# Optimization experiments

Hardware: AMD Instinct MI355X
Metric: run time of the kernel (lower is better)

The kernel has to match this reference:

```python
import jax, jax.numpy as jnp
import numpy as np

D_MODEL = 64
D_INNER = 128
D_STATE = 16
D_CONV = 4
DT_RANK = 4
P_PIX = 5
HH = 120
WW = 120


def _layernorm(x, g, b):
    m = x.mean(-1, keepdims=True)
    v = ((x - m) ** 2).mean(-1, keepdims=True)
    return (x - m) * jax.lax.rsqrt(v + 1e-5) * g + b


def _ssm_scan(delta, Bm, Cm, u, A):
    # delta,u: (b,L,d); Bm,Cm: (b,L,n); A: (d,n)
    def step(h, inp):
        dt, bt, ct, ut = inp  # (b,d),(b,n),(b,n),(b,d)
        h = h * jnp.exp(dt[:, :, None] * A) + (dt * ut)[:, :, None] * bt[:, None, :]
        return h, jnp.einsum('bdn,bn->bd', h, ct)
    h0 = jnp.zeros((u.shape[0], A.shape[0], A.shape[1]), u.dtype)
    xs = (jnp.swapaxes(delta, 0, 1), jnp.swapaxes(Bm, 0, 1),
          jnp.swapaxes(Cm, 0, 1), jnp.swapaxes(u, 0, 1))
    _, ys = jax.lax.scan(step, h0, xs)
    return jnp.swapaxes(ys, 0, 1)  # (b,L,d)


def _mamba(p, x):
    # faithful mamba_ssm Mamba with use_fast_path=False, out_proj=Identity
    in_w, conv_w, conv_b, xproj_w, dt_w, dt_b, A_log, Dv = p
    L = x.shape[1]
    xz = jnp.einsum('bld,ed->ble', x, in_w)  # (b,L,2*d_inner)
    xh, z = xz[..., :D_INNER], xz[..., D_INNER:]
    xp = jnp.pad(xh, ((0, 0), (D_CONV - 1, 0), (0, 0)))  # causal depthwise conv
    conv = conv_b + sum(xp[:, i:i + L, :] * conv_w[:, i] for i in range(D_CONV))
    xh = jax.nn.silu(conv)
    dbl = jnp.einsum('bld,ed->ble', xh, xproj_w)
    dt = dbl[..., :DT_RANK]
    Bm = dbl[..., DT_RANK:DT_RANK + D_STATE]
    Cm = dbl[..., DT_RANK + D_STATE:]
    delta = jax.nn.softplus(jnp.einsum('blr,dr->bld', dt, dt_w) + dt_b)
    A = -jnp.exp(A_log)
    y = _ssm_scan(delta, Bm, Cm, xh, A) + xh * Dv
    return y * jax.nn.silu(z)


def _bidir(p2, xn):
    inp = jnp.stack([xn, xn[:, ::-1]])  # forward + flipped sequence
    ys = jax.vmap(_mamba, in_axes=(0, 0))(p2, inp)
    return ys[0], ys[1]


def _pixel(x, p2, g, b, out_w):
    B, C, Hh, Ww = x.shape
    p = P_PIX
    NH, NW = Hh // p, Ww // p
    L = NH * NW
    xd = x.reshape(B, C, NH, p, NW, p).transpose(0, 3, 5, 1, 2, 4).reshape(B * p * p, C, L)
    xn = _layernorm(jnp.swapaxes(xd, 1, 2), g, b)
    yf, yb = _bidir(p2, xn)
    yo = jnp.einsum('bld,cd->blc', yf + yb[:, ::-1], out_w)
    xo = jnp.swapaxes(yo, 1, 2).reshape(B, p, p, C, NH, NW).transpose(0, 3, 4, 1, 5, 2).reshape(B, C, Hh, Ww)
    return xo + x


def _window(x, p2, g, b, out_w, out_bw):
    # window p==1: AvgPool(1)/Upsample(1) are identities
    B, C, Hh, Ww = x.shape
    L = Hh * Ww
    xn = _layernorm(jnp.swapaxes(x.reshape(B, C, L), 1, 2), g, b)
    yf, yb = _bidir(p2, xn)
    xM = jnp.einsum('bld,cd->bcl', yf, out_w)
    yM = jnp.einsum('bld,cd->bcl', yb, out_bw)
    xo = jnp.einsum('bld,cd->blc', yf + yb[:, ::-1], out_w)
    return jnp.swapaxes(xo, 1, 2).reshape(B, C, Hh, Ww) + x, xM, yM


def _edges(M, step=32):
    hub = np.arange(0, M, step)
    ii, jj = np.meshgrid(hub, hub, indexing='ij')
    mask = ii != jj
    # off-diagonal hub-hub edges + self loops for every node (GCNConv add_remaining_self_loops)
    src = np.concatenate([ii[mask], np.arange(M)])
    dst = np.concatenate([jj[mask], np.arange(M)])
    deg = np.bincount(dst, minlength=M).astype(np.float32)
    norm = (deg[src] ** -0.5) * (deg[dst] ** -0.5)
    return jnp.asarray(src), jnp.asarray(dst), jnp.asarray(norm, jnp.float32)


def _gcn(x, Wm, bv, src, dst, norm, M):
    h = jnp.einsum('bmf,gf->bmg', x, Wm)
    msg = h[:, src, :] * norm[None, :, None]          # (B,E,g)
    agg = jax.ops.segment_sum(jnp.swapaxes(msg, 0, 1), dst, num_segments=M)
    return jnp.swapaxes(agg, 0, 1) + bv


def setup_inputs() -> dict:
    key = jax.random.key(0)
    ks = iter(jax.random.split(key, 48))
    def rn(shape, scale=1.0):
        return jax.random.normal(next(ks), shape, jnp.float32) * scale
    d = {}
    d['x'] = rn((1, D_MODEL, HH, WW))
    for pre in ('pix', 'win'):
        d[pre + '_in_w'] = rn((4, 2, 2 * D_INNER, D_MODEL), D_MODEL ** -0.5)
        d[pre + '_conv_w'] = rn((4, 2, D_INNER, D_CONV), 0.3)
        d[pre + '_conv_b'] = rn((4, 2, D_INNER), 0.02)
        d[pre + '_xproj_w'] = rn((4, 2, DT_RANK + 2 * D_STATE, D_INNER), D_INNER ** -0.5)
        d[pre + '_dt_w'] = rn((4, 2, D_INNER, DT_RANK), DT_RANK ** -0.5)
        d[pre + '_dt_b'] = jax.random.uniform(next(ks), (4, 2, D_INNER), jnp.float32, -5.0, -3.0)
        d[pre + '_A_log'] = jnp.log(jax.random.uniform(next(ks), (4, 2, D_INNER, D_STATE), jnp.float32, 1.0, 16.0))
        d[pre + '_D'] = rn((4, 2, D_INNER), 0.5)
        d[pre + '_ln_g'] = jnp.ones((4, D_MODEL), jnp.float32)
        d[pre + '_ln_b'] = jnp.zeros((4, D_MODEL), jnp.float32)
    d['pix_out_w'] = rn((4, D_MODEL, D_INNER), D_INNER ** -0.5)
    d['win_out_w'] = rn((4, D_MODEL, D_INNER), D_INNER ** -0.5)
    d['win_out_bw'] = rn((4, D_MODEL, D_INNER), D_INNER ** -0.5)
    d['gcn_w1'] = rn((2 * D_MODEL, 4 * D_MODEL), (4 * D_MODEL) ** -0.5)
    d['gcn_b1'] = jnp.zeros((2 * D_MODEL,), jnp.float32)
    d['gcn_w2'] = rn((D_MODEL, 2 * D_MODEL), (2 * D_MODEL) ** -0.5)
    d['gcn_b2'] = jnp.zeros((D_MODEL,), jnp.float32)
    return d


def reference(x, pix_in_w, pix_conv_w, pix_conv_b, pix_xproj_w, pix_dt_w, pix_dt_b, pix_A_log, pix_D,
              win_in_w, win_conv_w, win_conv_b, win_xproj_w, win_dt_w, win_dt_b, win_A_log, win_D,
              pix_ln_g, pix_ln_b, win_ln_g, win_ln_b, pix_out_w, win_out_w, win_out_bw,
              gcn_w1, gcn_b1, gcn_w2, gcn_b2):
    pix_stack = (pix_in_w, pix_conv_w, pix_conv_b, pix_xproj_w, pix_dt_w, pix_dt_b, pix_A_log, pix_D)
    win_stack = (win_in_w, win_conv_w, win_conv_b, win_xproj_w, win_dt_w, win_dt_b, win_A_log, win_D)
    def pick(stack, i):
        return tuple(t[i] for t in stack)
    def branch(x0, base):
        lastx, xM, yM = x0, None, None
        for s in range(2):
            i = base + s
            a = _pixel(lastx, pick(pix_stack, i), pix_ln_g[i], pix_ln_b[i], pix_out_w[i])
            a, xM, yM = _window(a, pick(win_stack, i), win_ln_g[i], win_ln_b[i], win_out_w[i], win_out_bw[i])
            lastx = lastx + a
        return lastx, xM, yM
    old = x
    lastx, xM, yM = branch(x, 0)
    lastx_T, xMT, yMT = branch(jnp.swapaxes(x, 2, 3), 2)
    B, C, Hh, Ww = x.shape
    M = Hh * Ww
    nf = jnp.swapaxes(jnp.concatenate([xM, yM, xMT, yMT], axis=1), 1, 2)  # (B,M,4C)
    src, dst, norm = _edges(M)
    h = jax.nn.relu(_gcn(nf, gcn_w1, gcn_b1, src, dst, norm, M))
    g = _gcn(h, gcn_w2, gcn_b2, src, dst, norm, M)
    gcn_x = jnp.swapaxes(g, 1, 2).reshape(B, C, Hh, Ww)
    return gcn_x + old + lastx + jnp.swapaxes(lastx_T, 2, 3)
```

## Files before the change

### kernel.cpp

```cpp
#include <hip/hip_runtime.h>
#include <hip/hip_bf16.h>

#define MT 14400
#define WNC 150
#define WCL 96
#define PT 16

typedef unsigned short u16;

__device__ __forceinline__ float b2f(u16 u){
  union { unsigned int i; float f; } v; v.i = ((unsigned int)u) << 16; return v.f;
}
__device__ __forceinline__ u16 f2b(float f){
  union { unsigned int i; float f; } v; v.f = f;
  unsigned int x = v.i;
  return (u16)((x + 0x7fffu + ((x >> 16) & 1u)) >> 16);
}
__device__ __forceinline__ float siluf(float x){ return x / (1.f + expf(-x)); }
__device__ __forceinline__ float softplusf(float x){ return (x > 20.f) ? x : log1pf(expf(x)); }

__global__ __launch_bounds__(256) void k_detect(const u16* __restrict__ a, int n, int* __restrict__ flag){
  __shared__ int found;
  if (threadIdx.x == 0) found = 0;
  __syncthreads();
  int f = 0;
  for (int i = threadIdx.x; i < n; i += 256){
    float v = b2f(a[i]);
    if (!(fabsf(v) <= 1e9f)) f = 1;
  }
  if (f) atomicOr(&found, 1);
  __syncthreads();
// ... 43 lines not shown
  for (int c = 0; c < 64; c++)
    acc += W[(size_t)c * 128 + kk] * G1[(size_t)f * 256 + str * 64 + c];
  W1c[((size_t)str * 128 + kk) * 128 + f] = acc;
}

__global__ __launch_bounds__(256) void k_cvt_x(const void* __restrict__ x, float* __restrict__ imgA,
                                               const int* __restrict__ flag){
  int idx = blockIdx.x * 256 + threadIdx.x;
  int l = idx % MT, c = idx / MT;
  float v = (*flag) ? ((const float*)x)[idx] : b2f(((const u16*)x)[idx]);
  imgA[idx] = v;
  imgA[(size_t)64 * MT + (size_t)c * MT + (l % 120) * 120 + l / 120] = v;
}

__global__ __launch_bounds__(256) void k_prep_xn(const float* __restrict__ img, const float* __restrict__ lng,
                                                 const float* __restrict__ lnb, float* __restrict__ xn,
                                                 int s, int pixelMode){
  int tid = threadIdx.x;
  int q = blockIdx.x * 4 + (tid >> 6);
  int c = tid & 63;
  int g = q / MT, t = q % MT;
  int hw;
  if (pixelMode){
    int b = t / 576, l = t % 576;
    int ph = b / 5, pw = b % 5, nh = l / 24, nw = l % 24;
    hw = (nh * 5 + ph) * 120 + (nw * 5 + pw);
  } else hw = t;
  float v = img[(size_t)g * 64 * MT + (size_t)c * MT + hw];
  float sm = v;
  #pragma unroll
  for (int m = 32; m >= 1; m >>= 1) sm += __shfl_xor(sm, m);
  float mean = sm * (1.f / 64.f);
  float dv = v - mean;
  float s2 = dv * dv;
  #pragma unroll
  for (int m = 32; m >= 1; m >>= 1) s2 += __shfl_xor(s2, m);
  float var = s2 * (1.f / 64.f);
  int i2 = g * 2 + s;
  float o = dv * rsqrtf(var + 1e-5f) * lng[i2 * 64 + c] + lnb[i2 * 64 + c];
  xn[(size_t)g * MT * 64 + (size_t)t * 64 + c] = o;
}

__global__ __launch_bounds__(256) void k_inproj(const float* __restrict__ xn, const float* __restrict__ WT,
                                                float* __restrict__ xh, float* __restrict__ z,
                                                int s, int pixelMode){
  int gd = blockIdx.y, g = gd >> 1, dir = gd & 1;
  int i2 = (g * 2 + s) * 2 + dir;
  int ttile = blockIdx.x >> 1, ntile = blockIdx.x & 1;
  int t0 = ttile * 64;
  const float* WTm = WT + (size_t)i2 * 16384 + ntile * 128;

  __shared__ __align__(16) float sA[64 * 68];
  __shared__ __align__(16) float sB[64 * 128];
  int tid = threadIdx.x;

  {
    int k0 = (tid & 15) * 4;
    #pragma unroll
    for (int it = 0; it < 4; it++){
      int t = (tid >> 4) + it * 16;
      int tq = t0 + t, src = tq;
      if (dir){
        if (pixelMode){ int b = tq / 576, l = tq % 576; src = b * 576 + 575 - l; }
        else src = MT - 1 - tq;
      }
      float4 v = *(const float4*)&xn[(size_t)g * MT * 64 + (size_t)src * 64 + k0];
      *(float4*)&sA[t * 68 + k0] = v;
    }
  }
  {
    #pragma unroll
    for (int it = 0; it < 8; it++){
      int idx = it * 256 + tid;
      int k = idx >> 5, e4 = (idx & 31) * 4;
      float4 v = *(const float4*)&WTm[(size_t)k * 256 + e4];
      *(float4*)&sB[k * 128 + e4] = v;
    }
  }
  __syncthreads();

  int tr = tid >> 4, tc = tid & 15;
  float acc[4][8];
// ... 9 lines not shown
    #pragma unroll
    for (int kk = 0; kk < 4; kk++){
      float4 b0 = *(const float4*)&sB[(k0 + kk) * 128 + tc * 8];
      float4 b1 = *(const float4*)&sB[(k0 + kk) * 128 + tc * 8 + 4];
      float bv[8] = {b0.x, b0.y, b0.z, b0.w, b1.x, b1.y, b1.z, b1.w};
      #pragma unroll
      for (int i = 0; i < 4; i++){
        const float* ap = (const float*)&a4[i];
        float av = ap[kk];
        #pragma unroll
        for (int j = 0; j < 8; j++) acc[i][j] += av * bv[j];
      }
    }
  }

  float* dst = ntile ? z : xh;
  #pragma unroll
  for (int i = 0; i < 4; i++){
    int t_out = t0 + tr * 4 + i;
    size_t base = (size_t)gd * MT * 128 + (size_t)t_out * 128 + tc * 8;
    *(float4*)&dst[base]     = make_float4(acc[i][0], acc[i][1], acc[i][2], acc[i][3]);
    *(float4*)&dst[base + 4] = make_float4(acc[i][4], acc[i][5], acc[i][6], acc[i][7]);
  }
}

__global__ __launch_bounds__(256) void k_conv(const float* __restrict__ raw, const float* __restrict__ cw,
                                              const float* __restrict__ cb, float* __restrict__ xhs,
                                              int s, int pixelMode){
  int gd = blockIdx.y, g = gd >> 1, dir = gd & 1;
  int i2 = (g * 2 + s) * 2 + dir;
  int idx = blockIdx.x * 256 + threadIdx.x;
  int t = idx >> 7, ch = idx & 127;
  int SL = pixelMode ? 576 : MT;
  int pos = t % SL;
  const float* src = raw + (size_t)gd * MT * 128;
  const float* wrow = cw + (size_t)(i2 * 128 + ch) * 4;
  float acc = cb[i2 * 128 + ch];
  #pragma unroll
  for (int i = 0; i < 4; i++){
    int d = 3 - i;
    if (pos >= d) acc += src[(size_t)(t - d) * 128 + ch] * wrow[i];
  }
  xhs[(size_t)gd * MT * 128 + idx] = siluf(acc);
}

__global__ __launch_bounds__(256) void k_xproj(const float* __restrict__ xhs, const float* __restrict__ xpb,
                                               const float* __restrict__ dtw, const float* __restrict__ dtb,
                                               float* __restrict__ delta, float* __restrict__ Bm,
                                               float* __restrict__ Cm, int s){
  int gd = blockIdx.y, g = gd >> 1, dir = gd & 1;
  int i2 = (g * 2 + s) * 2 + dir;
  const float* XP = xpb + (size_t)i2 * 36 * 128;
  const float* DW = dtw + (size_t)i2 * 128 * 4;
  const float* DB = dtb + (size_t)i2 * 128;
  int t0 = blockIdx.x * 64;
  size_t gb = (size_t)gd * MT * 128;
  size_t gb16 = (size_t)gd * MT * 16;

  __shared__ __align__(16) float sX[64 * 132];
  __shared__ __align__(16) float sW[48 * 132];
  float* sDbl = sX;
  int tid = threadIdx.x;

  #pragma unroll
  for (int it = 0; it < 8; it++){
    int idx = it * 256 + tid;
    int tok = idx >> 5, k4 = (idx & 31) * 4;
    *(float4*)&sX[tok * 132 + k4] = *(const float4*)&xhs[gb + (size_t)(t0 + tok) * 128 + k4];
  }
  for (int idx = tid; idx < 48 * 32; idx += 256){
    int out = idx >> 5, k4 = (idx & 31) * 4;
    float4 v = (out < 36) ? *(const float4*)&XP[(size_t)out * 128 + k4]
                          : make_float4(0.f, 0.f, 0.f, 0.f);
    *(float4*)&sW[out * 132 + k4] = v;
  }
  __syncthreads();

  int tr = tid >> 4, tc = tid & 15;
  float acc[4][3];
  #pragma unroll
  for (int i = 0; i < 4; i++){ acc[i][0]=0.f; acc[i][1]=0.f; acc[i][2]=0.f; }

  for (int k0 = 0; k0 < 128; k0 += 4){
// ... 21 lines not shown
      int out = tc * 3 + j;
      if (out < 36) sDbl[(tr * 4 + i) * 52 + out] = acc[i][j];
    }
  }
  __syncthreads();

  {
    int d = tid & 127, half = tid >> 7;
    float4 dw = *(const float4*)&DW[(size_t)d * 4];
    float db = DB[d];
    #pragma unroll
    for (int it = 0; it < 32; it++){
      int t = it * 2 + half;
      const float* row = &sDbl[t * 52];
      float v = db + row[0] * dw.x + row[1] * dw.y + row[2] * dw.z + row[3] * dw.w;
      delta[gb + (size_t)(t0 + t) * 128 + d] = softplusf(v);
    }
  }
  #pragma unroll
  for (int it = 0; it < 8; it++){
    int flat = it * 256 + tid;
    int t = flat >> 5, n = flat & 31;
    float v = sDbl[t * 52 + 4 + n];
    if (n < 16) Bm[gb16 + (size_t)(t0 + t) * 16 + n] = v;
    else        Cm[gb16 + (size_t)(t0 + t) * 16 + (n - 16)] = v;
  }
}

__global__ __launch_bounds__(256) void k_scan_p1(const float* __restrict__ delta, const float* __restrict__ xhs,
                                                 const float* __restrict__ Bm, const float* __restrict__ A2b,
                                                 float* __restrict__ Acar, float* __restrict__ Bcar, int s){
  int gd = blockIdx.y, g = gd >> 1, dir = gd & 1;
  int i2 = (g * 2 + s) * 2 + dir;
  int chunk = blockIdx.x;
  int tid = threadIdx.x, ch = tid >> 1, nb = (tid & 1) * 8;
  float A2[8], ap[8], bc[8];
  #pragma unroll
  for (int j = 0; j < 8; j++){
    A2[j] = A2b[((size_t)i2 * 128 + ch) * 16 + nb + j];
    ap[j] = 1.f; bc[j] = 0.f;
  }
  size_t so = (size_t)gd * MT * 128 + (size_t)chunk * WCL * 128;
  size_t bo = (size_t)gd * MT * 16  + (size_t)chunk * WCL * 16;
  __shared__ __align__(16) float sd[PT * 128];
  __shared__ __align__(16) float su[PT * 128];
  __shared__ __align__(16) float sb[PT * 16];
  float4 rd0, rd1, ru0, ru1; float rb;
  {
    const float4* d4 = (const float4*)(delta + so);
    const float4* u4 = (const float4*)(xhs + so);
    rd0 = d4[2 * tid]; rd1 = d4[2 * tid + 1];
    ru0 = u4[2 * tid]; ru1 = u4[2 * tid + 1];
    rb = (Bm + bo)[tid];
  }
  const int NT = WCL / PT;
  for (int tile = 0; tile < NT; tile++){
    __syncthreads();
    ((float4*)sd)[2 * tid] = rd0; ((float4*)sd)[2 * tid + 1] = rd1;
    ((float4*)su)[2 * tid] = ru0; ((float4*)su)[2 * tid + 1] = ru1;
    sb[tid] = rb;
    __syncthreads();
    if (tile + 1 < NT){
      const float4* d4 = (const float4*)(delta + so + (size_t)(tile + 1) * PT * 128);
      const float4* u4 = (const float4*)(xhs + so + (size_t)(tile + 1) * PT * 128);
      rd0 = d4[2 * tid]; rd1 = d4[2 * tid + 1];
      ru0 = u4[2 * tid]; ru1 = u4[2 * tid + 1];
      rb = (Bm + bo + (size_t)(tile + 1) * PT * 16)[tid];
    }
    #pragma unroll
    for (int t = 0; t < PT; t++){
      float dt = sd[t * 128 + ch];
      float u  = su[t * 128 + ch];
      float du = dt * u;
      #pragma unroll
      for (int j = 0; j < 8; j++){
        float e = exp2f(dt * A2[j]);
        bc[j] = bc[j] * e + du * sb[t * 16 + nb + j];
        ap[j] *= e;
      }
    }
  }
  size_t o = ((size_t)gd * WNC + chunk) * 2048 + (size_t)ch * 16 + nb;
// ... 8 lines not shown
__global__ __launch_bounds__(256) void k_scan_p2(const float* __restrict__ Acar, const float* __restrict__ Bcar,
                                                 float* __restrict__ Hin, int resetPeriod){
  int flat = blockIdx.x * 256 + threadIdx.x;
  int cs = flat & 2047, gd = flat >> 11;
  float h = 0.f;
  int cnt = 0;
  for (int c = 0; c < WNC; c++){
    if (cnt == resetPeriod) { h = 0.f; cnt = 0; }
    cnt++;
    size_t o = ((size_t)gd * WNC + c) * 2048 + cs;
    Hin[o] = h;
    h = Acar[o] * h + Bcar[o];
  }
}

__global__ __launch_bounds__(256) void k_scan_p3(const float* __restrict__ delta, const float* __restrict__ xhs,
                                                 const float* __restrict__ Bm, const float* __restrict__ Cm,
                                                 const float* __restrict__ zz, const float* __restrict__ A2b,
                                                 const float* __restrict__ Db, const float* __restrict__ Hin,
                                                 float* __restrict__ ys, int s){
  int gd = blockIdx.y, g = gd >> 1, dir = gd & 1;
  int i2 = (g * 2 + s) * 2 + dir;
  int chunk = blockIdx.x;
  int tid = threadIdx.x, ch = tid >> 1, nb = (tid & 1) * 8;
  float A2[8], h[8];
  size_t ho = ((size_t)gd * WNC + chunk) * 2048 + (size_t)ch * 16 + nb;
  {
    const float4* H4 = (const float4*)(Hin + ho);
    float4 h0 = H4[0], h1 = H4[1];
    h[0]=h0.x; h[1]=h0.y; h[2]=h0.z; h[3]=h0.w;
    h[4]=h1.x; h[5]=h1.y; h[6]=h1.z; h[7]=h1.w;
  }
  #pragma unroll
  for (int j = 0; j < 8; j++) A2[j] = A2b[((size_t)i2 * 128 + ch) * 16 + nb + j];
  float Dv = Db[(size_t)i2 * 128 + ch];
  size_t so = (size_t)gd * MT * 128 + (size_t)chunk * WCL * 128;
  size_t bo = (size_t)gd * MT * 16  + (size_t)chunk * WCL * 16;
  __shared__ __align__(16) float sd[PT * 128];
  __shared__ __align__(16) float su[PT * 128];
  __shared__ __align__(16) float sb[PT * 16];
  __shared__ __align__(16) float sc[PT * 16];
  __shared__ __align__(16) float sy[PT * 128];
  float4 rd0, rd1, ru0, ru1; float rb, rc;
  {
    const float4* d4 = (const float4*)(delta + so);
    const float4* u4 = (const float4*)(xhs + so);
    rd0 = d4[2 * tid]; rd1 = d4[2 * tid + 1];
    ru0 = u4[2 * tid]; ru1 = u4[2 * tid + 1];
    rb = (Bm + bo)[tid]; rc = (Cm + bo)[tid];
  }
  const int NT = WCL / PT;
  for (int tile = 0; tile < NT; tile++){
    __syncthreads();
    ((float4*)sd)[2 * tid] = rd0; ((float4*)sd)[2 * tid + 1] = rd1;
    ((float4*)su)[2 * tid] = ru0; ((float4*)su)[2 * tid + 1] = ru1;
    sb[tid] = rb; sc[tid] = rc;
    __syncthreads();
    if (tile + 1 < NT){
      const float4* d4 = (const float4*)(delta + so + (size_t)(tile + 1) * PT * 128);
      const float4* u4 = (const float4*)(xhs + so + (size_t)(tile + 1) * PT * 128);
      rd0 = d4[2 * tid]; rd1 = d4[2 * tid + 1];
      ru0 = u4[2 * tid]; ru1 = u4[2 * tid + 1];
      rb = (Bm + bo + (size_t)(tile + 1) * PT * 16)[tid];
      rc = (Cm + bo + (size_t)(tile + 1) * PT * 16)[tid];
    }
    #pragma unroll
    for (int t = 0; t < PT; t++){
      float dt = sd[t * 128 + ch];
      float u  = su[t * 128 + ch];
      float du = dt * u;
      float acc = 0.f;
      #pragma unroll
      for (int j = 0; j < 8; j++){
        float e = exp2f(dt * A2[j]);
        h[j] = h[j] * e + du * sb[t * 16 + nb + j];
        acc += h[j] * sc[t * 16 + nb + j];
      }
      acc += __shfl_xor(acc, 1);
      if (!(tid & 1)) sy[t * 128 + ch] = acc + u * Dv;
    }
    __syncthreads();
    {
      const float4* z4 = (const float4*)(zz + so + (size_t)tile * PT * 128);
      float4* y4 = (float4*)(ys + so + (size_t)tile * PT * 128);
      #pragma unroll
      for (int i = 0; i < 2; i++){
        int f = 2 * tid + i;
        float4 yv = ((float4*)sy)[f];
        float4 zv = z4[f];
        yv.x *= siluf(zv.x); yv.y *= siluf(zv.y); yv.z *= siluf(zv.z); yv.w *= siluf(zv.w);
        y4[f] = yv;
      }
    }
    __syncthreads();
  }
}

__global__ __launch_bounds__(256) void k_outproj_pixel(const float* __restrict__ ys, const float* __restrict__ owb,
                                                       const float* __restrict__ imgA, float* __restrict__ imgB, int s){
  int g = blockIdx.y;
  int i2 = g * 2 + s;
  int tile = blockIdx.x;
  int t0 = tile * 64;
  int b = tile / 9, l0 = (tile % 9) * 64;
  const float* W = owb + (size_t)(i2 * 64) * 128;
  const float* Yf = ys + (size_t)(g * 2 + 0) * MT * 128;
  const float* Yb = ys + (size_t)(g * 2 + 1) * MT * 128;
  __shared__ __align__(16) float sA[64 * 36];
  __shared__ __align__(16) float sW[32 * 68];
  __shared__ __align__(16) float sO[64 * 68];
  int tid = threadIdx.x;
  int tr = tid >> 4, tc = tid & 15;
  float acc[4][4];
  #pragma unroll
  for (int i = 0; i < 4; i++){ acc[i][0]=0.f; acc[i][1]=0.f; acc[i][2]=0.f; acc[i][3]=0.f; }

  for (int kt = 0; kt < 4; kt++){
    int k0 = kt * 32;
    {
      int t = tid >> 2, f8 = (tid & 3) * 8;
      int rt = b * 576 + 575 - (l0 + t);
      const float4* pf = (const float4*)&Yf[(size_t)(t0 + t) * 128 + k0 + f8];
      const float4* pb = (const float4*)&Yb[(size_t)rt * 128 + k0 + f8];
      float4 v0 = pf[0], v1 = pf[1], w0 = pb[0], w1 = pb[1];
      v0.x += w0.x; v0.y += w0.y; v0.z += w0.z; v0.w += w0.w;
      v1.x += w1.x; v1.y += w1.y; v1.z += w1.z; v1.w += w1.w;
      *(float4*)&sA[t * 36 + f8] = v0; *(float4*)&sA[t * 36 + f8 + 4] = v1;
    }
    {
      int c = tid >> 2, f8 = (tid & 3) * 8;
      const float* wr = &W[(size_t)c * 128 + k0 + f8];
      #pragma unroll
      for (int j = 0; j < 8; j++) sW[(f8 + j) * 68 + c] = wr[j];
    }
    __syncthreads();
    #pragma unroll
    for (int k4 = 0; k4 < 32; k4 += 4){
      float4 a[4];
      #pragma unroll
      for (int i = 0; i < 4; i++) a[i] = *(const float4*)&sA[(tr * 4 + i) * 36 + k4];
      #pragma unroll
      for (int kk = 0; kk < 4; kk++){
// ... 14 lines not shown
  __syncthreads();
  {
    int c = tid >> 2, q = tid & 3;
    int ph = b / 5, pw = b % 5;
    size_t base = (size_t)g * 64 * MT + (size_t)c * MT;
    #pragma unroll
    for (int v = 0; v < 16; v++){
      int l = l0 + q * 16 + v;
      int nh = l / 24, nw = l % 24;
      size_t io = base + (nh * 5 + ph) * 120 + (nw * 5 + pw);
      imgB[io] = imgA[io] + sO[c * 68 + q * 16 + v];
    }
  }
}

__global__ __launch_bounds__(256) void k_outproj_win(const float* __restrict__ ys, const float* __restrict__ owb,
                                                     float* __restrict__ imgA, float* __restrict__ imgB, int s){
  int g = blockIdx.y;
  int i2 = g * 2 + s;
  int t0 = blockIdx.x * 64;
  const float* W = owb + (size_t)(i2 * 64) * 128;
  const float* Yf = ys + (size_t)(g * 2 + 0) * MT * 128;
  const float* Yb = ys + (size_t)(g * 2 + 1) * MT * 128;
  __shared__ __align__(16) float sA[64 * 36];
  __shared__ __align__(16) float sW[32 * 68];
  __shared__ __align__(16) float sO[64 * 68];
  int tid = threadIdx.x;
  int tr = tid >> 4, tc = tid & 15;
  float acc[4][4];
  #pragma unroll
  for (int i = 0; i < 4; i++){ acc[i][0]=0.f; acc[i][1]=0.f; acc[i][2]=0.f; acc[i][3]=0.f; }

  for (int kt = 0; kt < 4; kt++){
    int k0 = kt * 32;
    {
      int t = tid >> 2, f8 = (tid & 3) * 8;
      int l = t0 + t;
      const float4* pf = (const float4*)&Yf[(size_t)l * 128 + k0 + f8];
      const float4* pb = (const float4*)&Yb[(size_t)(MT - 1 - l) * 128 + k0 + f8];
      float4 v0 = pf[0], v1 = pf[1], w0 = pb[0], w1 = pb[1];
      v0.x += w0.x; v0.y += w0.y; v0.z += w0.z; v0.w += w0.w;
      v1.x += w1.x; v1.y += w1.y; v1.z += w1.z; v1.w += w1.w;
      *(float4*)&sA[t * 36 + f8] = v0; *(float4*)&sA[t * 36 + f8 + 4] = v1;
    }
    {
      int c = tid >> 2, f8 = (tid & 3) * 8;
      const float* wr = &W[(size_t)c * 128 + k0 + f8];
      #pragma unroll
      for (int j = 0; j < 8; j++) sW[(f8 + j) * 68 + c] = wr[j];
    }
    __syncthreads();
    #pragma unroll
    for (int k4 = 0; k4 < 32; k4 += 4){
      float4 a[4];
      #pragma unroll
      for (int i = 0; i < 4; i++) a[i] = *(const float4*)&sA[(tr * 4 + i) * 36 + k4];
      #pragma unroll
      for (int kk = 0; kk < 4; kk++){
// ... 19 lines not shown
    float* pA = &imgA[base];
    const float* pS = &sO[c * 68 + q * 16];
    #pragma unroll
    for (int v = 0; v < 4; v++){
      float4 d = *(const float4*)&pS[v * 4];
      float4 bb = *(const float4*)&pB[v * 4];
      bb.x += d.x; bb.y += d.y; bb.z += d.z; bb.w += d.w;
      *(float4*)&pB[v * 4] = bb;
      float4 aa = *(const float4*)&pA[v * 4];
      aa.x += bb.x; aa.y += bb.y; aa.z += bb.z; aa.w += bb.w;
      *(float4*)&pA[v * 4] = aa;
    }
  }
}

__global__ __launch_bounds__(256) void k_gcn1(const float* __restrict__ ys, const float* __restrict__ W1c,
                                              float* __restrict__ t1){
  int t0 = blockIdx.x * 64;
  __shared__ __align__(16) float sA[64 * 36];
  __shared__ __align__(16) float sB[32 * 132];
  int tid = threadIdx.x, tr = tid >> 4, tc = tid & 15;
  float acc[4][8];
  #pragma unroll
  for (int i = 0; i < 4; i++)
    #pragma unroll
    for (int j = 0; j < 8; j++) acc[i][j] = 0.f;

  for (int kt = 0; kt < 16; kt++){
    int str = kt >> 2, k0 = (kt & 3) * 32;
    const float* Y = ys + (size_t)str * MT * 128;
    {
      int t = tid >> 2, f8 = (tid & 3) * 8;
      const float4* p = (const float4*)&Y[(size_t)(t0 + t) * 128 + k0 + f8];
      *(float4*)&sA[t * 36 + f8] = p[0]; *(float4*)&sA[t * 36 + f8 + 4] = p[1];
    }
    {
      const float* Wc = W1c + ((size_t)str * 128 + k0) * 128;
      int kk = tid >> 3, f16 = (tid & 7) * 16;
      #pragma unroll
      for (int v = 0; v < 4; v++)
        *(float4*)&sB[kk * 132 + f16 + v * 4] = *(const float4*)&Wc[(size_t)kk * 128 + f16 + v * 4];
    }
    __syncthreads();
    #pragma unroll
    for (int k4 = 0; k4 < 32; k4 += 4){
      float4 a[4];
      #pragma unroll
      for (int i = 0; i < 4; i++) a[i] = *(const float4*)&sA[(tr * 4 + i) * 36 + k4];
      #pragma unroll
// ... 113 lines not shown
  if (n_in < 28 || in_sizes[I_PIW] != 131072 || out_size != 921600) return;

  float* Wp = (float*)d_ws;
  size_t off = 0;
  auto alloc = [&](size_t n){ size_t r = off; off += (n + 63) & ~(size_t)63; return r; };
  size_t oFlag=alloc(64);
  size_t oPIW=alloc(131072), oPCW=alloc(4096), oPCB=alloc(1024), oPXP=alloc(36864),
         oPDTW=alloc(4096), oPDTB=alloc(1024), oPA=alloc(16384), oPD=alloc(1024),
         oPLG=alloc(256), oPLB=alloc(256);
  size_t oWIW=alloc(131072), oWCW=alloc(4096), oWCB=alloc(1024), oWXP=alloc(36864),
         oWDTW=alloc(4096), oWDTB=alloc(1024), oWA=alloc(16384), oWD=alloc(1024),
         oWLG=alloc(256), oWLB=alloc(256);
  size_t oPOW=alloc(32768), oWOW=alloc(32768), oWOBW=alloc(32768),
         oG1=alloc(32768), oGB1=alloc(128), oG2=alloc(8192), oGB2=alloc(64);
  size_t oPIWT=alloc(131072), oWIWT=alloc(131072), oW1C=alloc(65536);
  size_t oImgA=alloc(2UL*64*MT), oImgB=alloc(2UL*64*MT), oXn=alloc(2UL*MT*64);
  size_t oRaw=alloc(4UL*MT*128);
  size_t oZ=alloc(4UL*MT*128), oXhs=alloc(4UL*MT*128), oDelta=alloc(4UL*MT*128);
  size_t oBm=alloc(4UL*MT*16), oCm=alloc(4UL*MT*16);
  size_t oAc=alloc(4UL*WNC*2048), oBc=alloc(4UL*WNC*2048), oHin=alloc(4UL*WNC*2048);
  size_t oT1=alloc((size_t)MT*128), oHub1=alloc(128), oT2=alloc((size_t)MT*64), oHub2=alloc(64);
  if (ws_size < off * sizeof(float)) return;

  int* flag = (int*)(Wp + oFlag);
  k_detect<<<dim3(1), dim3(256), 0, stream>>>((const u16*)d_in[I_PAL], 16384, flag);

  PTab tb;
  int ti = 0;
  auto add = [&](int inIdx, size_t o, int n, int neg){
    tb.src[ti] = d_in[inIdx]; tb.dst[ti] = Wp + o; tb.n[ti] = n; tb.neg[ti] = neg; ti++;
  };
  add(I_PIW,oPIW,131072,0); add(I_PCW,oPCW,4096,0); add(I_PCB,oPCB,1024,0); add(I_PXP,oPXP,36864,0);
  add(I_PDTW,oPDTW,4096,0); add(I_PDTB,oPDTB,1024,0); add(I_PAL,oPA,16384,1); add(I_PD,oPD,1024,0);
  add(I_PLG,oPLG,256,0); add(I_PLB,oPLB,256,0);
  add(I_WIW,oWIW,131072,0); add(I_WCW,oWCW,4096,0); add(I_WCB,oWCB,1024,0); add(I_WXP,oWXP,36864,0);
  add(I_WDTW,oWDTW,4096,0); add(I_WDTB,oWDTB,1024,0); add(I_WAL,oWA,16384,1); add(I_WD,oWD,1024,0);
  add(I_WLG,oWLG,256,0); add(I_WLB,oWLB,256,0);
  add(I_POW,oPOW,32768,0); add(I_WOW,oWOW,32768,0); add(I_WOBW,oWOBW,32768,0);
  add(I_G1,oG1,32768,0); add(I_GB1,oGB1,128,0); add(I_G2,oG2,8192,0); add(I_GB2,oGB2,64,0);

  k_cvt<<<dim3(128, 27), dim3(256), 0, stream>>>(tb, flag);
  k_wtrans<<<dim3(64, 16), dim3(256), 0, stream>>>(Wp+oPIW, Wp+oWIW, Wp+oPIWT, Wp+oWIWT);
  k_gcn1w<<<dim3(64, 4), dim3(256), 0, stream>>>(Wp+oWOW, Wp+oWOBW, Wp+oG1, Wp+oW1C);
  k_cvt_x<<<dim3(3600), dim3(256), 0, stream>>>(d_in[I_X], Wp + oImgA, flag);

  float *imgA = Wp+oImgA, *imgB = Wp+oImgB, *xn = Wp+oXn, *raw = Wp+oRaw, *ys = Wp+oRaw,
        *zz = Wp+oZ, *xhs = Wp+oXhs, *delta = Wp+oDelta, *Bm = Wp+oBm, *Cm = Wp+oCm,
        *Ac = Wp+oAc, *Bc = Wp+oBc, *Hin = Wp+oHin;

  for (int s = 0; s < 2; s++){
    k_prep_xn<<<dim3(7200), dim3(256), 0, stream>>>(imgA, Wp+oPLG, Wp+oPLB, xn, s, 1);
    k_inproj <<<dim3(450, 4), dim3(256), 0, stream>>>(xn, Wp+oPIWT, raw, zz, s, 1);
    k_conv   <<<dim3(7200, 4), dim3(256), 0, stream>>>(raw, Wp+oPCW, Wp+oPCB, xhs, s, 1);
    k_xproj  <<<dim3(225, 4), dim3(256), 0, stream>>>(xhs, Wp+oPXP, Wp+oPDTW, Wp+oPDTB, delta, Bm, Cm, s);
    k_scan_p1<<<dim3(WNC, 4), dim3(256), 0, stream>>>(delta, xhs, Bm, Wp+oPA, Ac, Bc, s);
    k_scan_p2<<<dim3(32), dim3(256), 0, stream>>>(Ac, Bc, Hin, 6);
    k_scan_p3<<<dim3(WNC, 4), dim3(256), 0, stream>>>(delta, xhs, Bm, Cm, zz, Wp+oPA, Wp+oPD, Hin, ys, s);
    k_outproj_pixel<<<dim3(225, 2), dim3(256), 0, stream>>>(ys, Wp+oPOW, imgA, imgB, s);

    k_prep_xn<<<dim3(7200), dim3(256), 0, stream>>>(imgB, Wp+oWLG, Wp+oWLB, xn, s, 0);
    k_inproj <<<dim3(450, 4), dim3(256), 0, stream>>>(xn, Wp+oWIWT, raw, zz, s, 0);
    k_conv   <<<dim3(7200, 4), dim3(256), 0, stream>>>(raw, Wp+oWCW, Wp+oWCB, xhs, s, 0);
    k_xproj  <<<dim3(225, 4), dim3(256), 0, stream>>>(xhs, Wp+oWXP, Wp+oWDTW, Wp+oWDTB, delta, Bm, Cm, s);
    k_scan_p1<<<dim3(WNC, 4), dim3(256), 0, stream>>>(delta, xhs, Bm, Wp+oWA, Ac, Bc, s);
    k_scan_p2<<<dim3(32), dim3(256), 0, stream>>>(Ac, Bc, Hin, WNC);
    k_scan_p3<<<dim3(WNC, 4), dim3(256), 0, stream>>>(delta, xhs, Bm, Cm, zz, Wp+oWA, Wp+oWD, Hin, ys, s);
    k_outproj_win<<<dim3(225, 2), dim3(256), 0, stream>>>(ys, Wp+oWOW, imgA, imgB, s);
  }

  k_gcn1<<<dim3(225), dim3(256), 0, stream>>>(ys, Wp+oW1C, Wp+oT1);
  k_hub1<<<dim3(1), dim3(128), 0, stream>>>(Wp+oT1, Wp+oHub1);
// ... 5 lines not shown
```

Before: 1.353 ms.

## Store Mamba intermediates as bf16 and double scan chunk count

Converts the large intermediate activations (normalized input, in-projection outputs, conv output, delta, B/C, scan outputs) from fp32 to bf16 storage, with fp32 compute kept inside kernels. This halves the memory traffic of these bandwidth-bound elementwise, projection and scan kernels. It also halves the scan chunk length and doubles the number of chunks to expose more parallelism in the chunked scan, at the cost of more carry work in the sequential combine pass. bf16 rounding of delta, B, C and the scan outputs adds numerical error.

Measured after the change: 1.332 ms. No clear change (-1.5%).

```diff
diff --git a/kernel.cpp b/kernel.cpp
--- a/kernel.cpp
+++ b/kernel.cpp
@@ -2,8 +2,8 @@
 #include <hip/hip_bf16.h>
 
 #define MT 14400
-#define WNC 150
-#define WCL 96
+#define WNC 300
+#define WCL 48
 #define PT 16
 
 typedef unsigned short u16;
@@ -15,6 +15,13 @@
   union { unsigned int i; float f; } v; v.f = f;
   unsigned int x = v.i;
   return (u16)((x + 0x7fffu + ((x >> 16) & 1u)) >> 16);
+}
+__device__ __forceinline__ unsigned int pk2(float a, float b){
+  return (unsigned int)f2b(a) | ((unsigned int)f2b(b) << 16);
+}
+__device__ __forceinline__ void st8(float* p, uint4 v){
+  *(float4*)p = make_float4(b2f((u16)v.x), b2f((u16)(v.x >> 16)), b2f((u16)v.y), b2f((u16)(v.y >> 16)));
+  *(float4*)(p + 4) = make_float4(b2f((u16)v.z), b2f((u16)(v.z >> 16)), b2f((u16)v.w), b2f((u16)(v.w >> 16)));
 }
 __device__ __forceinline__ float siluf(float x){ return x / (1.f + expf(-x)); }
 __device__ __forceinline__ float softplusf(float x){ return (x > 20.f) ? x : log1pf(expf(x)); }
@@ -88,7 +95,7 @@
 }
 
 __global__ __launch_bounds__(256) void k_prep_xn(const float* __restrict__ img, const float* __restrict__ lng,
-                                                 const float* __restrict__ lnb, float* __restrict__ xn,
+                                                 const float* __restrict__ lnb, u16* __restrict__ xn,
                                                  int s, int pixelMode){
   int tid = threadIdx.x;
   int q = blockIdx.x * 4 + (tid >> 6);
@@ -112,11 +119,11 @@
   float var = s2 * (1.f / 64.f);
   int i2 = g * 2 + s;
   float o = dv * rsqrtf(var + 1e-5f) * lng[i2 * 64 + c] + lnb[i2 * 64 + c];
-  xn[(size_t)g * MT * 64 + (size_t)t * 64 + c] = o;
-}
-
-__global__ __launch_bounds__(256) void k_inproj(const float* __restrict__ xn, const float* __restrict__ WT,
-                                                float* __restrict__ xh, float* __restrict__ z,
+  xn[(size_t)g * MT * 64 + (size_t)t * 64 + c] = f2b(o);
+}
+
+__global__ __launch_bounds__(256) void k_inproj(const u16* __restrict__ xn, const float* __restrict__ WT,
+                                                u16* __restrict__ xh, u16* __restrict__ z,
                                                 int s, int pixelMode){
   int gd = blockIdx.y, g = gd >> 1, dir = gd & 1;
   int i2 = (g * 2 + s) * 2 + dir;
@@ -138,8 +145,11 @@
         if (pixelMode){ int b = tq / 576, l = tq % 576; src = b * 576 + 575 - l; }
         else src = MT - 1 - tq;
       }
-      float4 v = *(const float4*)&xn[(size_t)g * MT * 64 + (size_t)src * 64 + k0];
-      *(float4*)&sA[t * 68 + k0] = v;
+      uint2 v = *(const uint2*)&xn[(size_t)g * MT * 64 + (size_t)src * 64 + k0];
+      sA[t * 68 + k0]     = b2f((u16)v.x);
+      sA[t * 68 + k0 + 1] = b2f((u16)(v.x >> 16));
+      sA[t * 68 + k0 + 2] = b2f((u16)v.y);
+      sA[t * 68 + k0 + 3] = b2f((u16)(v.y >> 16));
     }
   }
   {
@@ -179,18 +189,20 @@
     }
   }
 
-  float* dst = ntile ? z : xh;
+  u16* dst = ntile ? z : xh;
   #pragma unroll
   for (int i = 0; i < 4; i++){
     int t_out = t0 + tr * 4 + i;
     size_t base = (size_t)gd * MT * 128 + (size_t)t_out * 128 + tc * 8;
-    *(float4*)&dst[base]     = make_float4(acc[i][0], acc[i][1], acc[i][2], acc[i][3]);
-    *(float4*)&dst[base + 4] = make_float4(acc[i][4], acc[i][5], acc[i][6], acc[i][7]);
-  }
-}
-
-__global__ __launch_bounds__(256) void k_conv(const float* __restrict__ raw, const float* __restrict__ cw,
-                                              const float* __restrict__ cb, float* __restrict__ xhs,
+    uint4 o;
+    o.x = pk2(acc[i][0], acc[i][1]); o.y = pk2(acc[i][2], acc[i][3]);
+    o.z = pk2(acc[i][4], acc[i][5]); o.w = pk2(acc[i][6], acc[i][7]);
+    *(uint4*)&dst[base] = o;
+  }
+}
+
+__global__ __launch_bounds__(256) void k_conv(const u16* __restrict__ raw, const float* __restrict__ cw,
+                                              const float* __restrict__ cb, u16* __restrict__ xhs,
                                               int s, int pixelMode){
   int gd = blockIdx.y, g = gd >> 1, dir = gd & 1;
   int i2 = (g * 2 + s) * 2 + dir;
@@ -198,21 +210,21 @@
   int t = idx >> 7, ch = idx & 127;
   int SL = pixelMode ? 576 : MT;
   int pos = t % SL;
-  const float* src = raw + (size_t)gd * MT * 128;
+  const u16* src = raw + (size_t)gd * MT * 128;
   const float* wrow = cw + (size_t)(i2 * 128 + ch) * 4;
   float acc = cb[i2 * 128 + ch];
   #pragma unroll
   for (int i = 0; i < 4; i++){
     int d = 3 - i;
-    if (pos >= d) acc += src[(size_t)(t - d) * 128 + ch] * wrow[i];
-  }
-  xhs[(size_t)gd * MT * 128 + idx] = siluf(acc);
-}
-
-__global__ __launch_bounds__(256) void k_xproj(const float* __restrict__ xhs, const float* __restrict__ xpb,
+    if (pos >= d) acc += b2f(src[(size_t)(t - d) * 128 + ch]) * wrow[i];
+  }
+  xhs[(size_t)gd * MT * 128 + idx] = f2b(siluf(acc));
+}
+
+__global__ __launch_bounds__(256) void k_xproj(const u16* __restrict__ xhs, const float* __restrict__ xpb,
                                                const float* __restrict__ dtw, const float* __restrict__ dtb,
-                                               float* __restrict__ delta, float* __restrict__ Bm,
-                                               float* __restrict__ Cm, int s){
+                                               u16* __restrict__ delta, u16* __restrict__ Bm,
+                                               u16* __restrict__ Cm, int s){
   int gd = blockIdx.y, g = gd >> 1, dir = gd & 1;
   int i2 = (g * 2 + s) * 2 + dir;
   const float* XP = xpb + (size_t)i2 * 36 * 128;
@@ -231,7 +243,11 @@
   for (int it = 0; it < 8; it++){
     int idx = it * 256 + tid;
     int tok = idx >> 5, k4 = (idx & 31) * 4;
-    *(float4*)&sX[tok * 132 + k4] = *(const float4*)&xhs[gb + (size_t)(t0 + tok) * 128 + k4];
+    uint2 v = *(const uint2*)&xhs[gb + (size_t)(t0 + tok) * 128 + k4];
+    sX[tok * 132 + k4]     = b2f((u16)v.x);
+    sX[tok * 132 + k4 + 1] = b2f((u16)(v.x >> 16));
+    sX[tok * 132 + k4 + 2] = b2f((u16)v.y);
+    sX[tok * 132 + k4 + 3] = b2f((u16)(v.y >> 16));
   }
   for (int idx = tid; idx < 48 * 32; idx += 256){
     int out = idx >> 5, k4 = (idx & 31) * 4;
@@ -283,7 +299,7 @@
       int t = it * 2 + half;
       const float* row = &sDbl[t * 52];
       float v = db + row[0] * dw.x + row[1] * dw.y + row[2] * dw.z + row[3] * dw.w;
-      delta[gb + (size_t)(t0 + t) * 128 + d] = softplusf(v);
+      delta[gb + (size_t)(t0 + t) * 128 + d] = f2b(softplusf(v));
     }
   }
   #pragma unroll
@@ -291,13 +307,13 @@
     int flat = it * 256 + tid;
     int t = flat >> 5, n = flat & 31;
     float v = sDbl[t * 52 + 4 + n];
-    if (n < 16) Bm[gb16 + (size_t)(t0 + t) * 16 + n] = v;
-    else        Cm[gb16 + (size_t)(t0 + t) * 16 + (n - 16)] = v;
-  }
-}
-
-__global__ __launch_bounds__(256) void k_scan_p1(const float* __restrict__ delta, const float* __restrict__ xhs,
-                                                 const float* __restrict__ Bm, const float* __restrict__ A2b,
+    if (n < 16) Bm[gb16 + (size_t)(t0 + t) * 16 + n] = f2b(v);
+    else        Cm[gb16 + (size_t)(t0 + t) * 16 + (n - 16)] = f2b(v);
+  }
+}
+
+__global__ __launch_bounds__(256) void k_scan_p1(const u16* __restrict__ delta, const u16* __restrict__ xhs,
+                                                 const u16* __restrict__ Bm, const float* __restrict__ A2b,
                                                  float* __restrict__ Acar, float* __restrict__ Bcar, int s){
   int gd = blockIdx.y, g = gd >> 1, dir = gd & 1;
   int i2 = (g * 2 + s) * 2 + dir;
@@ -314,27 +330,21 @@
   __shared__ __align__(16) float sd[PT * 128];
   __shared__ __align__(16) float su[PT * 128];
   __shared__ __align__(16) float sb[PT * 16];
-  float4 rd0, rd1, ru0, ru1; float rb;
-  {
-    const float4* d4 = (const float4*)(delta + so);
-    const float4* u4 = (const float4*)(xhs + so);
-    rd0 = d4[2 * tid]; rd1 = d4[2 * tid + 1];
-    ru0 = u4[2 * tid]; ru1 = u4[2 * tid + 1];
-    rb = (Bm + bo)[tid];
-  }
+  uint4 rd, ru; float rbf;
+  rd = *(const uint4*)&delta[so + 8 * (size_t)tid];
+  ru = *(const uint4*)&xhs[so + 8 * (size_t)tid];
+  rbf = b2f(Bm[bo + tid]);
   const int NT = WCL / PT;
   for (int tile = 0; tile < NT; tile++){
     __syncthreads();
-    ((float4*)sd)[2 * tid] = rd0; ((float4*)sd)[2 * tid + 1] = rd1;
-    ((float4*)su)[2 * tid] = ru0; ((float4*)su)[2 * tid + 1] = ru1;
-    sb[tid] = rb;
+    st8(&sd[8 * tid], rd);
+    st8(&su[8 * tid], ru);
+    sb[tid] = rbf;
     __syncthreads();
     if (tile + 1 < NT){
-      const float4* d4 = (const float4*)(delta + so + (size_t)(tile + 1) * PT * 128);
-      const float4* u4 = (const float4*)(xhs + so + (size_t)(tile + 1) * PT * 128);
-      rd0 = d4[2 * tid]; rd1 = d4[2 * tid + 1];
-      ru0 = u4[2 * tid]; ru1 = u4[2 * tid + 1];
-      rb = (Bm + bo + (size_t)(tile + 1) * PT * 16)[tid];
+      rd = *(const uint4*)&delta[so + (size_t)(tile + 1) * PT * 128 + 8 * (size_t)tid];
+      ru = *(const uint4*)&xhs[so + (size_t)(tile + 1) * PT * 128 + 8 * (size_t)tid];
+      rbf = b2f(Bm[bo + (size_t)(tile + 1) * PT * 16 + tid]);
     }
     #pragma unroll
     for (int t = 0; t < PT; t++){
@@ -373,11 +383,11 @@
   }
 }
 
-__global__ __launch_bounds__(256) void k_scan_p3(const float* __restrict__ delta, const float* __restrict__ xhs,
-                                                 const float* __restrict__ Bm, const float* __restrict__ Cm,
-                                                 const float* __restrict__ zz, const float* __restrict__ A2b,
+__global__ __launch_bounds__(256) void k_scan_p3(const u16* __restrict__ delta, const u16* __restrict__ xhs,
+                                                 const u16* __restrict__ Bm, const u16* __restrict__ Cm,
+                                                 const u16* __restrict__ zz, const float* __restrict__ A2b,
                                                  const float* __restrict__ Db, const float* __restrict__ Hin,
-                                                 float* __restrict__ ys, int s){
+                                                 u16* __restrict__ ys, int s){
   int gd = blockIdx.y, g = gd >> 1, dir = gd & 1;
   int i2 = (g * 2 + s) * 2 + dir;
   int chunk = blockIdx.x;
@@ -400,28 +410,22 @@
   __shared__ __align__(16) float sb[PT * 16];
   __shared__ __align__(16) float sc[PT * 16];
   __shared__ __align__(16) float sy[PT * 128];
-  float4 rd0, rd1, ru0, ru1; float rb, rc;
-  {
-    const float4* d4 = (const float4*)(delta + so);
-    const float4* u4 = (const float4*)(xhs + so);
-    rd0 = d4[2 * tid]; rd1 = d4[2 * tid + 1];
-    ru0 = u4[2 * tid]; ru1 = u4[2 * tid + 1];
-    rb = (Bm + bo)[tid]; rc = (Cm + bo)[tid];
-  }
+  uint4 rd, ru; float rbf, rcf;
+  rd = *(const uint4*)&delta[so + 8 * (size_t)tid];
+  ru = *(const uint4*)&xhs[so + 8 * (size_t)tid];
+  rbf = b2f(Bm[bo + tid]); rcf = b2f(Cm[bo + tid]);
   const int NT = WCL / PT;
   for (int tile = 0; tile < NT; tile++){
     __syncthreads();
-    ((float4*)sd)[2 * tid] = rd0; ((float4*)sd)[2 * tid + 1] = rd1;
-    ((float4*)su)[2 * tid] = ru0; ((float4*)su)[2 * tid + 1] = ru1;
-    sb[tid] = rb; sc[tid] = rc;
+    st8(&sd[8 * tid], rd);
+    st8(&su[8 * tid], ru);
+    sb[tid] = rbf; sc[tid] = rcf;
     __syncthreads();
     if (tile + 1 < NT){
-      const float4* d4 = (const float4*)(delta + so + (size_t)(tile + 1) * PT * 128);
-      const float4* u4 = (const float4*)(xhs + so + (size_t)(tile + 1) * PT * 128);
-      rd0 = d4[2 * tid]; rd1 = d4[2 * tid + 1];
-      ru0 = u4[2 * tid]; ru1 = u4[2 * tid + 1];
-      rb = (Bm + bo + (size_t)(tile + 1) * PT * 16)[tid];
-      rc = (Cm + bo + (size_t)(tile + 1) * PT * 16)[tid];
+      rd = *(const uint4*)&delta[so + (size_t)(tile + 1) * PT * 128 + 8 * (size_t)tid];
+      ru = *(const uint4*)&xhs[so + (size_t)(tile + 1) * PT * 128 + 8 * (size_t)tid];
+      rbf = b2f(Bm[bo + (size_t)(tile + 1) * PT * 16 + tid]);
+      rcf = b2f(Cm[bo + (size_t)(tile + 1) * PT * 16 + tid]);
     }
     #pragma unroll
     for (int t = 0; t < PT; t++){
@@ -440,22 +444,22 @@
     }
     __syncthreads();
     {
-      const float4* z4 = (const float4*)(zz + so + (size_t)tile * PT * 128);
-      float4* y4 = (float4*)(ys + so + (size_t)tile * PT * 128);
-      #pragma unroll
-      for (int i = 0; i < 2; i++){
-        int f = 2 * tid + i;
-        float4 yv = ((float4*)sy)[f];
-        float4 zv = z4[f];
-        yv.x *= siluf(zv.x); yv.y *= siluf(zv.y); yv.z *= siluf(zv.z); yv.w *= siluf(zv.w);
-        y4[f] = yv;
-      }
-    }
-    __syncthreads();
-  }
-}
-
-__global__ __launch_bounds__(256) void k_outproj_pixel(const float* __restrict__ ys, const float* __restrict__ owb,
+      uint4 zv = *(const uint4*)&zz[so + (size_t)tile * PT * 128 + 8 * (size_t)tid];
+      const float* py = &sy[8 * tid];
+      float y[8];
+      y[0] = py[0] * siluf(b2f((u16)zv.x));       y[1] = py[1] * siluf(b2f((u16)(zv.x >> 16)));
+      y[2] = py[2] * siluf(b2f((u16)zv.y));       y[3] = py[3] * siluf(b2f((u16)(zv.y >> 16)));
+      y[4] = py[4] * siluf(b2f((u16)zv.z));       y[5] = py[5] * siluf(b2f((u16)(zv.z >> 16)));
+      y[6] = py[6] * siluf(b2f((u16)zv.w));       y[7] = py[7] * siluf(b2f((u16)(zv.w >> 16)));
+      uint4 o;
+      o.x = pk2(y[0], y[1]); o.y = pk2(y[2], y[3]); o.z = pk2(y[4], y[5]); o.w = pk2(y[6], y[7]);
+      *(uint4*)&ys[so + (size_t)tile * PT * 128 + 8 * (size_t)tid] = o;
+    }
+    __syncthreads();
+  }
+}
+
+__global__ __launch_bounds__(256) void k_outproj_pixel(const u16* __restrict__ ys, const float* __restrict__ owb,
                                                        const float* __restrict__ imgA, float* __restrict__ imgB, int s){
   int g = blockIdx.y;
   int i2 = g * 2 + s;
@@ -463,8 +467,8 @@
   int t0 = tile * 64;
   int b = tile / 9, l0 = (tile % 9) * 64;
   const float* W = owb + (size_t)(i2 * 64) * 128;
-  const float* Yf = ys + (size_t)(g * 2 + 0) * MT * 128;
-  const float* Yb = ys + (size_t)(g * 2 + 1) * MT * 128;
+  const u16* Yf = ys + (size_t)(g * 2 + 0) * MT * 128;
+  const u16* Yb = ys + (size_t)(g * 2 + 1) * MT * 128;
   __shared__ __align__(16) float sA[64 * 36];
   __shared__ __align__(16) float sW[32 * 68];
   __shared__ __align__(16) float sO[64 * 68];
@@ -479,12 +483,17 @@
     {
       int t = tid >> 2, f8 = (tid & 3) * 8;
       int rt = b * 576 + 575 - (l0 + t);
-      const float4* pf = (const float4*)&Yf[(size_t)(t0 + t) * 128 + k0 + f8];
-      const float4* pb = (const float4*)&Yb[(size_t)rt * 128 + k0 + f8];
-      float4 v0 = pf[0], v1 = pf[1], w0 = pb[0], w1 = pb[1];
-      v0.x += w0.x; v0.y += w0.y; v0.z += w0.z; v0.w += w0.w;
-      v1.x += w1.x; v1.y += w1.y; v1.z += w1.z; v1.w += w1.w;
-      *(float4*)&sA[t * 36 + f8] = v0; *(float4*)&sA[t * 36 + f8 + 4] = v1;
+      uint4 vf = *(const uint4*)&Yf[(size_t)(t0 + t) * 128 + k0 + f8];
+      uint4 vb = *(const uint4*)&Yb[(size_t)rt * 128 + k0 + f8];
+      float* pa = &sA[t * 36 + f8];
+      pa[0] = b2f((u16)vf.x) + b2f((u16)vb.x);
+      pa[1] = b2f((u16)(vf.x >> 16)) + b2f((u16)(vb.x >> 16));
+      pa[2] = b2f((u16)vf.y) + b2f((u16)vb.y);
+      pa[3] = b2f((u16)(vf.y >> 16)) + b2f((u16)(vb.y >> 16));
+      pa[4] = b2f((u16)vf.z) + b2f((u16)vb.z);
+      pa[5] = b2f((u16)(vf.z >> 16)) + b2f((u16)(vb.z >> 16));
+      pa[6] = b2f((u16)vf.w) + b2f((u16)vb.w);
+      pa[7] = b2f((u16)(vf.w >> 16)) + b2f((u16)(vb.w >> 16));
     }
     {
       int c = tid >> 2, f8 = (tid & 3) * 8;
@@ -529,14 +538,14 @@
   }
 }
 
-__global__ __launch_bounds__(256) void k_outproj_win(const float* __restrict__ ys, const float* __restrict__ owb,
+__global__ __launch_bounds__(256) void k_outproj_win(const u16* __restrict__ ys, const float* __restrict__ owb,
                                                      float* __restrict__ imgA, float* __restrict__ imgB, int s){
   int g = blockIdx.y;
   int i2 = g * 2 + s;
   int t0 = blockIdx.x * 64;
   const float* W = owb + (size_t)(i2 * 64) * 128;
-  const float* Yf = ys + (size_t)(g * 2 + 0) * MT * 128;
-  const float* Yb = ys + (size_t)(g * 2 + 1) * MT * 128;
+  const u16* Yf = ys + (size_t)(g * 2 + 0) * MT * 128;
+  const u16* Yb = ys + (size_t)(g * 2 + 1) * MT * 128;
   __shared__ __align__(16) float sA[64 * 36];
   __shared__ __align__(16) float sW[32 * 68];
   __shared__ __align__(16) float sO[64 * 68];
@@ -551,12 +560,17 @@
     {
       int t = tid >> 2, f8 = (tid & 3) * 8;
       int l = t0 + t;
-      const float4* pf = (const float4*)&Yf[(size_t)l * 128 + k0 + f8];
-      const float4* pb = (const float4*)&Yb[(size_t)(MT - 1 - l) * 128 + k0 + f8];
-      float4 v0 = pf[0], v1 = pf[1], w0 = pb[0], w1 = pb[1];
-      v0.x += w0.x; v0.y += w0.y; v0.z += w0.z; v0.w += w0.w;
-      v1.x += w1.x; v1.y += w1.y; v1.z += w1.z; v1.w += w1.w;
-      *(float4*)&sA[t * 36 + f8] = v0; *(float4*)&sA[t * 36 + f8 + 4] = v1;
+      uint4 vf = *(const uint4*)&Yf[(size_t)l * 128 + k0 + f8];
+      uint4 vb = *(const uint4*)&Yb[(size_t)(MT - 1 - l) * 128 + k0 + f8];
+      float* pa = &sA[t * 36 + f8];
+      pa[0] = b2f((u16)vf.x) + b2f((u16)vb.x);
+      pa[1] = b2f((u16)(vf.x >> 16)) + b2f((u16)(vb.x >> 16));
+      pa[2] = b2f((u16)vf.y) + b2f((u16)vb.y);
+      pa[3] = b2f((u16)(vf.y >> 16)) + b2f((u16)(vb.y >> 16));
+      pa[4] = b2f((u16)vf.z) + b2f((u16)vb.z);
+      pa[5] = b2f((u16)(vf.z >> 16)) + b2f((u16)(vb.z >> 16));
+      pa[6] = b2f((u16)vf.w) + b2f((u16)vb.w);
+      pa[7] = b2f((u16)(vf.w >> 16)) + b2f((u16)(vb.w >> 16));
     }
     {
       int c = tid >> 2, f8 = (tid & 3) * 8;
@@ -606,7 +620,7 @@
   }
 }
 
-__global__ __launch_bounds__(256) void k_gcn1(const float* __restrict__ ys, const float* __restrict__ W1c,
+__global__ __launch_bounds__(256) void k_gcn1(const u16* __restrict__ ys, const float* __restrict__ W1c,
                                               float* __restrict__ t1){
   int t0 = blockIdx.x * 64;
   __shared__ __align__(16) float sA[64 * 36];
@@ -620,11 +634,11 @@
 
   for (int kt = 0; kt < 16; kt++){
     int str = kt >> 2, k0 = (kt & 3) * 32;
-    const float* Y = ys + (size_t)str * MT * 128;
+    const u16* Y = ys + (size_t)str * MT * 128;
     {
       int t = tid >> 2, f8 = (tid & 3) * 8;
-      const float4* p = (const float4*)&Y[(size_t)(t0 + t) * 128 + k0 + f8];
-      *(float4*)&sA[t * 36 + f8] = p[0]; *(float4*)&sA[t * 36 + f8 + 4] = p[1];
+      uint4 p = *(const uint4*)&Y[(size_t)(t0 + t) * 128 + k0 + f8];
+      st8(&sA[t * 36 + f8], p);
     }
     {
       const float* Wc = W1c + ((size_t)str * 128 + k0) * 128;
@@ -768,10 +782,11 @@
   size_t oPOW=alloc(32768), oWOW=alloc(32768), oWOBW=alloc(32768),
          oG1=alloc(32768), oGB1=alloc(128), oG2=alloc(8192), oGB2=alloc(64);
   size_t oPIWT=alloc(131072), oWIWT=alloc(131072), oW1C=alloc(65536);
-  size_t oImgA=alloc(2UL*64*MT), oImgB=alloc(2UL*64*MT), oXn=alloc(2UL*MT*64);
-  size_t oRaw=alloc(4UL*MT*128);
-  size_t oZ=alloc(4UL*MT*128), oXhs=alloc(4UL*MT*128), oDelta=alloc(4UL*MT*128);
-  size_t oBm=alloc(4UL*MT*16), oCm=alloc(4UL*MT*16);
+  size_t oImgA=alloc(2UL*64*MT), oImgB=alloc(2UL*64*MT);
+  size_t oXn=alloc((size_t)MT*64);
+  size_t oRaw=alloc(2UL*MT*128);
+  size_t oZ=alloc(2UL*MT*128), oXhs=alloc(2UL*MT*128), oDelta=alloc(2UL*MT*128);
+  size_t oBm=alloc(2UL*MT*16), oCm=alloc(2UL*MT*16);
   size_t oAc=alloc(4UL*WNC*2048), oBc=alloc(4UL*WNC*2048), oHin=alloc(4UL*WNC*2048);
   size_t oT1=alloc((size_t)MT*128), oHub1=alloc(128), oT2=alloc((size_t)MT*64), oHub2=alloc(64);
   if (ws_size < off * sizeof(float)) return;
@@ -798,9 +813,11 @@
   k_gcn1w<<<dim3(64, 4), dim3(256), 0, stream>>>(Wp+oWOW, Wp+oWOBW, Wp+oG1, Wp+oW1C);
   k_cvt_x<<<dim3(3600), dim3(256), 0, stream>>>(d_in[I_X], Wp + oImgA, flag);
 
-  float *imgA = Wp+oImgA, *imgB = Wp+oImgB, *xn = Wp+oXn, *raw = Wp+oRaw, *ys = Wp+oRaw,
-        *zz = Wp+oZ, *xhs = Wp+oXhs, *delta = Wp+oDelta, *Bm = Wp+oBm, *Cm = Wp+oCm,
+  float *imgA = Wp+oImgA, *imgB = Wp+oImgB,
         *Ac = Wp+oAc, *Bc = Wp+oBc, *Hin = Wp+oHin;
+  u16 *xn = (u16*)(Wp+oXn), *raw = (u16*)(Wp+oRaw), *ys = (u16*)(Wp+oRaw),
+      *zz = (u16*)(Wp+oZ), *xhs = (u16*)(Wp+oXhs), *delta = (u16*)(Wp+oDelta),
+      *Bm = (u16*)(Wp+oBm), *Cm = (u16*)(Wp+oCm);
 
   for (int s = 0; s < 2; s++){
     k_prep_xn<<<dim3(7200), dim3(256), 0, stream>>>(imgA, Wp+oPLG, Wp+oPLB, xn, s, 1);
@@ -808,7 +825,7 @@
     k_conv   <<<dim3(7200, 4), dim3(256), 0, stream>>>(raw, Wp+oPCW, Wp+oPCB, xhs, s, 1);
     k_xproj  <<<dim3(225, 4), dim3(256), 0, stream>>>(xhs, Wp+oPXP, Wp+oPDTW, Wp+oPDTB, delta, Bm, Cm, s);
     k_scan_p1<<<dim3(WNC, 4), dim3(256), 0, stream>>>(delta, xhs, Bm, Wp+oPA, Ac, Bc, s);
-    k_scan_p2<<<dim3(32), dim3(256), 0, stream>>>(Ac, Bc, Hin, 6);
+    k_scan_p2<<<dim3(32), dim3(256), 0, stream>>>(Ac, Bc, Hin, 12);
     k_scan_p3<<<dim3(WNC, 4), dim3(256), 0, stream>>>(delta, xhs, Bm, Cm, zz, Wp+oPA, Wp+oPD, Hin, ys, s);
     k_outproj_pixel<<<dim3(225, 2), dim3(256), 0, stream>>>(ys, Wp+oPOW, imgA, imgB, s);
 
```
